# Optimization experiments

Hardware: AMD Instinct MI355X
Metric: run time of the kernel (lower is better)

The kernel has to match this reference:

```python
import jax, jax.numpy as jnp
import numpy as np

B, N, M = 8, 4096, 4096


def setup_inputs() -> dict:
    key = jax.random.key(0)
    k1, k2 = jax.random.split(key)
    tar = jax.random.normal(k1, (B, N, 3), dtype=jnp.float32)
    src = jax.random.normal(k2, (B, M, 3), dtype=jnp.float32)
    return {"tar": tar, "src": src}


def reference(tar, src):
    # diff: [b, n, m, 3]; dist: [b, n, m] Euclidean norm
    diff = tar[:, :, None, :] - src[:, None, :, :]
    dist = jnp.sqrt(jnp.sum(diff * diff, axis=-1))
    # complete: for each target point, min over source points, mean over n -> [b]
    complete = jnp.mean(jnp.min(dist, axis=2), axis=1)
    # accuracy: for each source point, min over target points, mean over m -> [b]
    accuracy = jnp.mean(jnp.min(dist, axis=1), axis=1)
    # reduction='mean' over batch axis
    complete = jnp.mean(complete, axis=-1)
    accuracy = jnp.mean(accuracy, axis=-1)
    chamfer = 0.5 * (complete + accuracy)
    return (accuracy, complete, chamfer)
```

## Files before the change

kernel.cpp:

```cpp
#include <hip/hip_runtime.h>
#include <math.h>

#define B_ 8

__global__ __launch_bounds__(256) void init_ws_kernel(unsigned int* ws, int n) {
    int i = blockIdx.x * 256 + threadIdx.x;
    if (i < n) ws[i] = 0x7F800000u;
}

template <int QPT, int CHUNK>
__global__ __launch_bounds__(256) void minsq_kernel(
    const float* __restrict__ tar, const float* __restrict__ src,
    unsigned int* __restrict__ ws, int N, int M)
{
    const int z   = blockIdx.z;
    const int dir = (z >= B_) ? 1 : 0;
    const int b   = dir ? (z - B_) : z;
    const float* __restrict__ qry = dir ? src : tar;
    const float* __restrict__ pts = dir ? tar : src;
    const int K = dir ? M : N;
    const int L = dir ? N : M;
    unsigned int* __restrict__ out =
        ws + (dir ? (size_t)B_ * N : (size_t)0) + (size_t)b * K;

    const int base = blockIdx.y * CHUNK;
    if (base >= L) return;
    const int cnt = min(CHUNK, L - base);

    __shared__ float4 sp[CHUNK];
    const float* __restrict__ psrc = pts + ((size_t)b * L + base) * 3;
    const int t = threadIdx.x;
    for (int i = t; i < cnt; i += 256) {
        float px = psrc[3 * i + 0];
        float py = psrc[3 * i + 1];
        float pz = psrc[3 * i + 2];
        float pw = fmaf(px, px, fmaf(py, py, pz * pz));
        sp[i] = make_float4(px, py, pz, pw);
    }
    __syncthreads();

    const int qbase = blockIdx.x * (256 * QPT);
    float qx2[QPT], qy2[QPT], qz2[QPT], qw[QPT], mn[QPT];
#pragma unroll
    for (int k = 0; k < QPT; ++k) {
        int qi = qbase + k * 256 + t;
        if (qi < K) {
            const float* qp = qry + ((size_t)b * K + qi) * 3;
            float x = qp[0], y = qp[1], zc = qp[2];
            qx2[k] = -2.f * x; qy2[k] = -2.f * y; qz2[k] = -2.f * zc;
            qw[k] = fmaf(x, x, fmaf(y, y, zc * zc));
        } else {
            qx2[k] = 0.f; qy2[k] = 0.f; qz2[k] = 0.f; qw[k] = 0.f;
        }
        mn[k] = 3.4e38f;
    }

    if (cnt == CHUNK) {
#pragma unroll 4
        for (int j = 0; j < CHUNK; ++j) {
            float4 p = sp[j];
#pragma unroll
            for (int k = 0; k < QPT; ++k) {
                float d2 = fmaf(qx2[k], p.x,
                           fmaf(qy2[k], p.y,
                           fmaf(qz2[k], p.z, p.w)));
                mn[k] = fminf(mn[k], d2);
            }
        }
    } else {
        for (int j = 0; j < cnt; ++j) {
            float4 p = sp[j];
#pragma unroll
            for (int k = 0; k < QPT; ++k) {
                float d2 = fmaf(qx2[k], p.x,
                           fmaf(qy2[k], p.y,
                           fmaf(qz2[k], p.z, p.w)));
                mn[k] = fminf(mn[k], d2);
            }
        }
    }

#pragma unroll
    for (int k = 0; k < QPT; ++k) {
        int qi = qbase + k * 256 + t;
        if (qi < K) {
            float d2 = fmaxf(mn[k] + qw[k], 0.f);
            atomicMin(&out[qi], __float_as_uint(d2));
        }
    }
}

__global__ __launch_bounds__(1024) void reduce_kernel(
    const unsigned int* __restrict__ ws, float* __restrict__ outp, int N, int M)
{
    const int t  = threadIdx.x;
    const int nt = B_ * N;
    const int ns = B_ * M;
    float s_t = 0.f, s_s = 0.f;
    for (int i = t; i < nt; i += 1024) s_t += sqrtf(__uint_as_float(ws[i]));
    for (int i = t; i < ns; i += 1024) s_s += sqrtf(__uint_as_float(ws[nt + i]));

#pragma unroll
    for (int off = 32; off > 0; off >>= 1) {
        s_t += __shfl_down(s_t, off);
        s_s += __shfl_down(s_s, off);
    }

    __shared__ float red_t[16], red_s[16];
    const int wid = t >> 6, lid = t & 63;
    if (lid == 0) { red_t[wid] = s_t; red_s[wid] = s_s; }
    __syncthreads();
    if (t == 0) {
        float ct = 0.f, ac = 0.f;
#pragma unroll
        for (int w = 0; w < 16; ++w) { ct += red_t[w]; ac += red_s[w]; }
        float complete = ct / (float)nt;
        float accuracy = ac / (float)ns;
        outp[0] = accuracy;
        outp[1] = complete;
        outp[2] = 0.5f * (accuracy + complete);
    }
}

extern "C" void kernel_launch(void* const* d_in, const int* in_sizes, int n_in,
                              void* d_out, int out_size, void* d_ws, size_t ws_size,
                              hipStream_t stream) {
    const float* tar = (const float*)d_in[0];
    const float* src = (const float*)d_in[1];
    const int N = in_sizes[0] / (B_ * 3);
    const int M = in_sizes[1] / (B_ * 3);
    unsigned int* ws = (unsigned int*)d_ws;

    const int tot = B_ * (N + M);
    init_ws_kernel<<<dim3((tot + 255) / 256), dim3(256), 0, stream>>>(ws, tot);

    constexpr int QPT = 8, CHUNK = 256;
    const int KL = (N > M) ? N : M;
    const int gx = (KL + 256 * QPT - 1) / (256 * QPT);
    const int gy = (KL + CHUNK - 1) / CHUNK;
    dim3 grid(gx, gy, 2 * B_);
    minsq_kernel<QPT, CHUNK><<<grid, dim3(256), 0, stream>>>(tar, src, ws, N, M);

    reduce_kernel<<<1, dim3(1024), 0, stream>>>(ws, (float*)d_out, N, M);
}
```

Measured before the change: 102.3 us.

## Split final reduction across blocks, pair-unroll inner loop, retune QPT/CHUNK

The single-block reduction is replaced by a 128-block partial-sum kernel followed by a tiny finalize kernel, so summing the 64K minima no longer sits on one workgroup. The inner distance loop now handles two source points per iteration and merges them with a nested fminf, which cuts the serial min dependency chain. The tiling moves from 8 queries per thread with 256-point chunks to 4 queries per thread with 512-point chunks, doubling the x-grid while halving the y-grid. The cost is one extra kernel launch and lower per-thread register reuse of each shared-memory load.

Result: faster. 85.50 us (-16.4%).

```diff
diff --git a/kernel.cpp b/kernel.cpp
--- a/kernel.cpp
+++ b/kernel.cpp
@@ -2,6 +2,7 @@
 #include <math.h>
 
 #define B_ 8
+
 
 __global__ __launch_bounds__(256) void init_ws_kernel(unsigned int* ws, int n) {
     int i = blockIdx.x * 256 + threadIdx.x;
@@ -34,8 +35,7 @@
         float px = psrc[3 * i + 0];
         float py = psrc[3 * i + 1];
         float pz = psrc[3 * i + 2];
-        float pw = fmaf(px, px, fmaf(py, py, pz * pz));
-        sp[i] = make_float4(px, py, pz, pw);
+        sp[i] = make_float4(px, py, pz, fmaf(px, px, fmaf(py, py, pz * pz)));
     }
     __syncthreads();
 
@@ -57,25 +57,44 @@
 
     if (cnt == CHUNK) {
 #pragma unroll 4
-        for (int j = 0; j < CHUNK; ++j) {
-            float4 p = sp[j];
+        for (int j = 0; j < CHUNK; j += 2) {
+            float4 p0 = sp[j];
+            float4 p1 = sp[j + 1];
 #pragma unroll
             for (int k = 0; k < QPT; ++k) {
-                float d2 = fmaf(qx2[k], p.x,
-                           fmaf(qy2[k], p.y,
-                           fmaf(qz2[k], p.z, p.w)));
-                mn[k] = fminf(mn[k], d2);
+                float d0 = fmaf(qx2[k], p0.x,
+                           fmaf(qy2[k], p0.y,
+                           fmaf(qz2[k], p0.z, p0.w)));
+                float d1 = fmaf(qx2[k], p1.x,
+                           fmaf(qy2[k], p1.y,
+                           fmaf(qz2[k], p1.z, p1.w)));
+                mn[k] = fminf(mn[k], fminf(d0, d1));
             }
         }
     } else {
-        for (int j = 0; j < cnt; ++j) {
-            float4 p = sp[j];
+        int j = 0;
+        for (; j + 1 < cnt; j += 2) {
+            float4 p0 = sp[j];
+            float4 p1 = sp[j + 1];
 #pragma unroll
             for (int k = 0; k < QPT; ++k) {
-                float d2 = fmaf(qx2[k], p.x,
-                           fmaf(qy2[k], p.y,
-                           fmaf(qz2[k], p.z, p.w)));
-                mn[k] = fminf(mn[k], d2);
+                float d0 = fmaf(qx2[k], p0.x,
+                           fmaf(qy2[k], p0.y,
+                           fmaf(qz2[k], p0.z, p0.w)));
+                float d1 = fmaf(qx2[k], p1.x,
+                           fmaf(qy2[k], p1.y,
+                           fmaf(qz2[k], p1.z, p1.w)));
+                mn[k] = fminf(mn[k], fminf(d0, d1));
+            }
+        }
+        if (j < cnt) {
+            float4 p0 = sp[j];
+#pragma unroll
+            for (int k = 0; k < QPT; ++k) {
+                float d0 = fmaf(qx2[k], p0.x,
+                           fmaf(qy2[k], p0.y,
+                           fmaf(qz2[k], p0.z, p0.w)));
+                mn[k] = fminf(mn[k], d0);
             }
         }
     }
@@ -90,32 +109,52 @@
     }
 }
 
-__global__ __launch_bounds__(1024) void reduce_kernel(
-    const unsigned int* __restrict__ ws, float* __restrict__ outp, int N, int M)
+__global__ __launch_bounds__(256) void reduce1_kernel(
+    const unsigned int* __restrict__ ws, float* __restrict__ partials,
+    int N, int M)
 {
-    const int t  = threadIdx.x;
     const int nt = B_ * N;
     const int ns = B_ * M;
+    const int gid = blockIdx.x * 256 + threadIdx.x;
+    const int stride = gridDim.x * 256;
     float s_t = 0.f, s_s = 0.f;
-    for (int i = t; i < nt; i += 1024) s_t += sqrtf(__uint_as_float(ws[i]));
-    for (int i = t; i < ns; i += 1024) s_s += sqrtf(__uint_as_float(ws[nt + i]));
+    for (int i = gid; i < nt; i += stride) s_t += sqrtf(__uint_as_float(ws[i]));
+    for (int i = gid; i < ns; i += stride) s_s += sqrtf(__uint_as_float(ws[nt + i]));
 
 #pragma unroll
     for (int off = 32; off > 0; off >>= 1) {
         s_t += __shfl_down(s_t, off);
         s_s += __shfl_down(s_s, off);
     }
+    __shared__ float rt[4], rs[4];
+    const int wid = threadIdx.x >> 6, lid = threadIdx.x & 63;
+    if (lid == 0) { rt[wid] = s_t; rs[wid] = s_s; }
+    __syncthreads();
+    if (threadIdx.x == 0) {
+        float a = rt[0] + rt[1] + rt[2] + rt[3];
+        float c = rs[0] + rs[1] + rs[2] + rs[3];
+        partials[blockIdx.x]       = a;
+        partials[128 + blockIdx.x] = c;
+    }
+}
 
-    __shared__ float red_t[16], red_s[16];
-    const int wid = t >> 6, lid = t & 63;
-    if (lid == 0) { red_t[wid] = s_t; red_s[wid] = s_s; }
+__global__ __launch_bounds__(128) void finalize_kernel(
+    const float* __restrict__ partials, float* __restrict__ outp, int N, int M)
+{
+    const int t = threadIdx.x;
+    float s_t = partials[t];
+    float s_s = partials[128 + t];
+#pragma unroll
+    for (int off = 32; off > 0; off >>= 1) {
+        s_t += __shfl_down(s_t, off);
+        s_s += __shfl_down(s_s, off);
+    }
+    __shared__ float rt[2], rs[2];
+    if ((t & 63) == 0) { rt[t >> 6] = s_t; rs[t >> 6] = s_s; }
     __syncthreads();
     if (t == 0) {
-        float ct = 0.f, ac = 0.f;
-#pragma unroll
-        for (int w = 0; w < 16; ++w) { ct += red_t[w]; ac += red_s[w]; }
-        float complete = ct / (float)nt;
-        float accuracy = ac / (float)ns;
+        float complete = (rt[0] + rt[1]) / (float)(B_ * N);
+        float accuracy = (rs[0] + rs[1]) / (float)(B_ * M);
         outp[0] = accuracy;
         outp[1] = complete;
         outp[2] = 0.5f * (accuracy + complete);
@@ -130,16 +169,18 @@
     const int N = in_sizes[0] / (B_ * 3);
     const int M = in_sizes[1] / (B_ * 3);
     unsigned int* ws = (unsigned int*)d_ws;
+    float* partials = (float*)(ws + (size_t)B_ * (N + M));
 
     const int tot = B_ * (N + M);
     init_ws_kernel<<<dim3((tot + 255) / 256), dim3(256), 0, stream>>>(ws, tot);
 
-    constexpr int QPT = 8, CHUNK = 256;
+    constexpr int QPT = 4, CHUNK = 512;
     const int KL = (N > M) ? N : M;
     const int gx = (KL + 256 * QPT - 1) / (256 * QPT);
     const int gy = (KL + CHUNK - 1) / CHUNK;
     dim3 grid(gx, gy, 2 * B_);
     minsq_kernel<QPT, CHUNK><<<grid, dim3(256), 0, stream>>>(tar, src, ws, N, M);
 
-    reduce_kernel<<<1, dim3(1024), 0, stream>>>(ws, (float*)d_out, N, M);
+    reduce1_kernel<<<dim3(128), dim3(256), 0, stream>>>(ws, partials, N, M);
+    finalize_kernel<<<dim3(1), dim3(128), 0, stream>>>(partials, (float*)d_out, N, M);
 }
```
